# Kernel tuning notes

Hardware: AMD Instinct MI355X
Metric: run time of the kernel (lower is better)

## Reference

```python
import jax, jax.numpy as jnp
import numpy as np

N_NODES = 50000
N_EDGES = 600000
NODE_DIM = 128
HID = 128
NUM_LAYERS = 3


def setup_inputs() -> dict:
    key = jax.random.key(0)
    ks = jax.random.split(key, 16)
    s = lambda fan_in: 1.0 / np.sqrt(fan_in)
    inp = {
        'node_features': jax.random.normal(ks[0], (N_NODES, NODE_DIM), dtype=jnp.float32),
        'edge_index': jax.random.randint(ks[1], (2, N_EDGES), 0, N_NODES, dtype=jnp.int64 if jax.config.jax_enable_x64 else jnp.int32),
        # node embedding
        'W_emb': jax.random.uniform(ks[2], (NODE_DIM, HID), jnp.float32, -s(NODE_DIM), s(NODE_DIM)),
        'b_emb': jnp.zeros((HID,), jnp.float32),
        # gnn layers (stacked over layer axis)
        'W_gnn': jax.random.uniform(ks[3], (NUM_LAYERS, HID, HID), jnp.float32, -s(HID), s(HID)),
        'b_gnn': jnp.zeros((NUM_LAYERS, HID), jnp.float32),
        # edge mask generator
        'W_m1': jax.random.uniform(ks[4], (2 * HID, HID), jnp.float32, -s(2 * HID), s(2 * HID)),
        'b_m1': jnp.zeros((HID,), jnp.float32),
        'W_m2': jax.random.uniform(ks[5], (HID, 1), jnp.float32, -s(HID), s(HID)),
        'b_m2': jnp.zeros((1,), jnp.float32),
        # predictor
        'W_p1': jax.random.uniform(ks[6], (HID, HID), jnp.float32, -s(HID), s(HID)),
        'b_p1': jnp.zeros((HID,), jnp.float32),
        'W_p2': jax.random.uniform(ks[7], (HID, 1), jnp.float32, -s(HID), s(HID)),
        'b_p2': jnp.zeros((1,), jnp.float32),
    }
    return inp


def _edge_mask(h, src, dst, W_m1, b_m1, W_m2, b_m2):
    # per-edge gather + concat -> 2-layer MLP -> sigmoid importance
    ef = jnp.concatenate([h[src], h[dst]], axis=1)          # [E, 2H]
    imp = jax.nn.sigmoid(jax.nn.relu(ef @ W_m1 + b_m1) @ W_m2 + b_m2)[:, 0]  # [E]
    # eval mode: temp=2.0, offset=0.4
    return jax.nn.sigmoid((imp - 0.4) * 2.0)


def reference(node_features, edge_index, W_emb, b_emb, W_gnn, b_gnn,
              W_m1, b_m1, W_m2, b_m2, W_p1, b_p1, W_p2, b_p2):
    src, dst = edge_index[0], edge_index[1]
    n = node_features.shape[0]
    h = jax.nn.relu(node_features @ W_emb + b_emb)           # [N, H]
    mask = _edge_mask(h, src, dst, W_m1, b_m1, W_m2, b_m2)    # [E]
    for i in range(NUM_LAYERS):
        msgs = jax.ops.segment_sum(h[src] * mask[:, None], dst, num_segments=n)  # scatter-add
        h = jax.nn.relu((h + msgs) @ W_gnn[i] + b_gnn[i])
        if i < NUM_LAYERS - 1:
            mask = _edge_mask(h, src, dst, W_m1, b_m1, W_m2, b_m2)
    prediction = jax.nn.relu(h[0] @ W_p1 + b_p1) @ W_p2 + b_p2  # [1]
    return prediction, mask, h
```

## Files before the change

kernel.cpp:

```cpp
#include <hip/hip_runtime.h>
#include <hip/hip_bf16.h>

#define NN 50000
#define NE 600000
#define HD 128
#define DET_SAMPLES 65536
#define NBLK 196
#define NTILES 3125
#define GPERS 782
#define LDT 136

typedef unsigned short ushort_t;
typedef __attribute__((ext_vector_type(8))) short short8v;
typedef __attribute__((ext_vector_type(4))) float f32x4;

__device__ __forceinline__ float sigmoidf_(float x){ return 1.f/(1.f+__expf(-x)); }

__device__ __forceinline__ ushort_t f2bf(float f){
  unsigned int u = __float_as_uint(f);
  unsigned int r = (u + 0x7FFFu + ((u >> 16) & 1u)) >> 16;
  return (ushort_t)r;
}

__device__ __forceinline__ float bflo(unsigned u){ return __uint_as_float(u << 16); }
__device__ __forceinline__ float bfhi(unsigned u){ return __uint_as_float(u & 0xFFFF0000u); }

__global__ void write_scalar_kernel(float* __restrict__ p, float v){ p[0] = v; }

__global__ void detect_kernel(const unsigned int* __restrict__ w, int* __restrict__ flag){
  int i = blockIdx.x*256 + threadIdx.x;
  int z = (w[2*i + 1] == 0u) ? 1 : 0;
  atomicAdd(flag, z);
}

__global__ void extract_kernel(const void* __restrict__ ei, const int* __restrict__ flag,
                               int* __restrict__ srcW, int* __restrict__ dstW,
                               int* __restrict__ counts){
  const int e = blockIdx.x*256 + threadIdx.x;
  if (e >= NE) return;
  int s, d;
  if (*flag > (DET_SAMPLES/2)){
    const long long* p = (const long long*)ei;
    s = (int)p[e]; d = (int)p[NE + e];
  } else {
    const int* p = (const int*)ei;
    s = p[e]; d = p[NE + e];
  }
  srcW[e] = s; dstW[e] = d;
  atomicAdd(&counts[d], 1);
}

__global__ __launch_bounds__(256) void scanA_kernel(const int* __restrict__ counts,
                                                    int* __restrict__ partial){
  __shared__ int s[256];
  const int t = threadIdx.x;
  const int idx = blockIdx.x*256 + t;
  s[t] = (idx < NN) ? counts[idx] : 0;
  __syncthreads();
  for (int off = 128; off > 0; off >>= 1){
    if (t < off) s[t] += s[t + off];
    __syncthreads();
  }
  if (t == 0) partial[blockIdx.x] = s[0];
}

__global__ __launch_bounds__(256) void scanB_kernel(const int* __restrict__ partial,
                                                    int* __restrict__ bOff){
  __shared__ int s[256];
  const int t = threadIdx.x;
  const int v = (t < NBLK) ? partial[t] : 0;
  s[t] = v;
  __syncthreads();
  for (int off = 1; off < 256; off <<= 1){
    int add = (t >= off) ? s[t - off] : 0;
    __syncthreads();
    s[t] += add;
    __syncthreads();
  }
  if (t < NBLK) bOff[t] = s[t] - v;
}

__global__ __launch_bounds__(256) void scanC_kernel(const int* __restrict__ counts,
    const int* __restrict__ bOff, int* __restrict__ row_start, int* __restrict__ cursor){
  __shared__ int s[256];
  const int t = threadIdx.x;
  const int idx = blockIdx.x*256 + t;
  const int c = (idx < NN) ? counts[idx] : 0;
  s[t] = c;
  __syncthreads();
  for (int off = 1; off < 256; off <<= 1){
    int add = (t >= off) ? s[t - off] : 0;
    __syncthreads();
    s[t] += add;
    __syncthreads();
  }
  const int excl = bOff[blockIdx.x] + s[t] - c;
  if (idx < NN){ row_start[idx] = excl; cursor[idx] = excl; }
  else if (idx == NN){ row_start[NN] = excl; }
}

__global__ void fill_kernel(const int* __restrict__ dstI, const int* __restrict__ srcI,
                            int* __restrict__ cursor, int* __restrict__ eids,
                            int* __restrict__ srcS){
  int e = blockIdx.x*256 + threadIdx.x;
  if (e < NE){
    int p = atomicAdd(&cursor[dstI[e]], 1);
    eids[p] = e;
    srcS[p] = srcI[e];
  }
}

__global__ __launch_bounds__(256) void wcvt_all_kernel(const float* __restrict__ Wemb,
    const float* __restrict__ Wgnn, const float* __restrict__ Wm1,
    ushort_t* __restrict__ WtAll){
  const int idx = blockIdx.x*256 + threadIdx.x;
  const int m = idx >> 14;
  const int r = idx & 16383;
  const int k = r >> 7, n = r & 127;
  const float* W = (m == 0) ? Wemb : (m <= 3) ? (Wgnn + (size_t)(m-1)*16384)
                                              : (Wm1  + (size_t)(m-4)*16384);
  WtAll[(size_t)m*16384 + n*HD + k] = f2bf(W[r]);
}

template<int F32A, int DOUV>
__global__ __launch_bounds__(256, 3) void gemm_fused(const void* __restrict__ inP,
    const ushort_t* __restrict__ Wt, const float* __restrict__ bias,
    float* __restrict__ outF, ushort_t* __restrict__ outB,
    const ushort_t* __restrict__ WtU, const ushort_t* __restrict__ WtV,
    const float* __restrict__ biasU, ushort_t* __restrict__ outU,
    ushort_t* __restrict__ outV)
{
  __shared__ ushort_t hT[16*LDT];
  const int cq   = threadIdx.x >> 6;
  const int lane = threadIdx.x & 63;
  const int fr = lane & 15;
  const int fq = lane >> 4;
  short8v bh[4][2];
  #pragma unroll
  for (int ks = 0; ks < 4; ++ks)
    #pragma unroll
    for (int tcl = 0; tcl < 2; ++tcl)
      bh[ks][tcl] = *(const short8v*)(Wt + (size_t)((cq*2+tcl)*16 + fr)*HD + ks*32 + fq*8);
  short8v bu[4][2], bv[4][2];
  if (DOUV){
    #pragma unroll
    for (int ks = 0; ks < 4; ++ks)
      #pragma unroll
      for (int tcl = 0; tcl < 2; ++tcl){
        bu[ks][tcl] = *(const short8v*)(WtU + (size_t)((cq*2+tcl)*16 + fr)*HD + ks*32 + fq*8);
        bv[ks][tcl] = *(const short8v*)(WtV + (size_t)((cq*2+tcl)*16 + fr)*HD + ks*32 + fq*8);
      }
  }
  float bb[2], bub[2];
  #pragma unroll
  for (int tcl = 0; tcl < 2; ++tcl){
    const int col = (cq*2 + tcl)*16 + fr;
    bb[tcl]  = bias ? bias[col] : 0.f;
    bub[tcl] = DOUV ? biasU[col] : 0.f;
  }

  for (int it = 0; it < 4; ++it){
    const int tile = blockIdx.x + it*GPERS;
    if (tile >= NTILES) break;
    const int row0 = tile*16;
    const int arow = row0 + fr;
    f32x4 acc0 = (f32x4)0.0f, acc1 = (f32x4)0.0f;
    #pragma unroll
    for (int ks = 0; ks < 4; ++ks){
      const int k0 = ks*32 + fq*8;
      short8v af;
      if (F32A){
        const float* in = (const float*)inP;
        const float4 a0 = *(const float4*)(in + (size_t)arow*HD + k0);
        const float4 a1 = *(const float4*)(in + (size_t)arow*HD + k0 + 4);
        af[0]=(short)f2bf(a0.x); af[1]=(short)f2bf(a0.y);
        af[2]=(short)f2bf(a0.z); af[3]=(short)f2bf(a0.w);
        af[4]=(short)f2bf(a1.x); af[5]=(short)f2bf(a1.y);
        af[6]=(short)f2bf(a1.z); af[7]=(short)f2bf(a1.w);
      } else {
        const ushort_t* inB = (const ushort_t*)inP;
        af = *(const short8v*)(inB + (size_t)arow*HD + k0);
      }
      acc0 = __builtin_amdgcn_mfma_f32_16x16x32_bf16(af, bh[ks][0], acc0, 0, 0, 0);
      acc1 = __builtin_amdgcn_mfma_f32_16x16x32_bf16(af, bh[ks][1], acc1, 0, 0, 0);
    }
    #pragma unroll
    for (int tcl = 0; tcl < 2; ++tcl){
      const f32x4 a = tcl ? acc1 : acc0;
      const int col = (cq*2 + tcl)*16 + fr;
      #pragma unroll
      for (int j = 0; j < 4; ++j){
        const int r = row0 + fq*4 + j;
        float x = a[j] + bb[tcl];
        x = fmaxf(x, 0.f);
        const ushort_t xb = f2bf(x);
        if (DOUV) hT[(fq*4 + j)*LDT + col] = xb;
        if (outF) outF[(size_t)r*HD + col] = x;
        if (outB) outB[(size_t)r*HD + col] = xb;
      }
    }
    if (DOUV){
      __syncthreads();
      f32x4 aU0 = (f32x4)0.0f, aU1 = (f32x4)0.0f;
      f32x4 aV0 = (f32x4)0.0f, aV1 = (f32x4)0.0f;
      #pragma unroll
      for (int ks = 0; ks < 4; ++ks){
        const short8v af = *(const short8v*)(hT + fr*LDT + ks*32 + fq*8);
        aU0 = __builtin_amdgcn_mfma_f32_16x16x32_bf16(af, bu[ks][0], aU0, 0, 0, 0);
        aU1 = __builtin_amdgcn_mfma_f32_16x16x32_bf16(af, bu[ks][1], aU1, 0, 0, 0);
        aV0 = __builtin_amdgcn_mfma_f32_16x16x32_bf16(af, bv[ks][0], aV0, 0, 0, 0);
        aV1 = __builtin_amdgcn_mfma_f32_16x16x32_bf16(af, bv[ks][1], aV1, 0, 0, 0);
      }
      #pragma unroll
      for (int tcl = 0; tcl < 2; ++tcl){
        const f32x4 u = tcl ? aU1 : aU0;
        const f32x4 v = tcl ? aV1 : aV0;
        const int col = (cq*2 + tcl)*16 + fr;
        #pragma unroll
        for (int j = 0; j < 4; ++j){
          const int r = row0 + fq*4 + j;
          outU[(size_t)r*HD + col] = f2bf(u[j] + bub[tcl]);
          outV[(size_t)r*HD + col] = f2bf(v[j]);
        }
      }
      __syncthreads();
    }
  }
}

__global__ __launch_bounds__(256) void mask_msg_kernel(
    const ushort_t* __restrict__ U, const ushort_t* __restrict__ V,
    const ushort_t* __restrict__ hB,
    ushort_t* __restrict__ hB2,
    const int* __restrict__ srcS, const int* __restrict__ eidS,
    const int* __restrict__ row_start,
    const float* __restrict__ Wm2, const float* __restrict__ bm2,
    float* __restrict__ maskOut)
{
  const int v = blockIdx.x*4 + (threadIdx.x >> 6);
  const int lane = threadIdx.x & 63;
  const int g   = lane >> 4;
  const int sub = lane & 15;
  const float4 wA = ((const float4*)Wm2)[sub*2];
  const float4 wB = ((const float4*)Wm2)[sub*2+1];
  const float b2 = bm2[0];
  const uint4 vv = ((const uint4*)(V + (size_t)v*HD))[sub];
  float a0=0.f,a1=0.f,a2=0.f,a3=0.f,a4=0.f,a5=0.f,a6=0.f,a7=0.f;
  const int beg = row_start[v], end = row_start[v+1];
  int idx = beg + g;
  uint4 uu = make_uint4(0,0,0,0), hh = make_uint4(0,0,0,0);
  int e0 = 0;
  if (idx < end){
    const int s = srcS[idx];
    if (maskOut) e0 = eidS[idx];
    uu = ((const uint4*)(U  + (size_t)s*HD))[sub];
    hh = ((const uint4*)(hB + (size_t)s*HD))[sub];
  }
  while (idx < end){
    const int nidx = idx + 4;
    uint4 uuN = make_uint4(0,0,0,0), hhN = make_uint4(0,0,0,0);
    int eN = 0;
    if (nidx < end){
      const int sn = srcS[nidx];
      if (maskOut) eN = eidS[nidx];
      uuN = ((const uint4*)(U  + (size_t)sn*HD))[sub];
      hhN = ((const uint4*)(hB + (size_t)sn*HD))[sub];
    }
    float p;
    p = fmaxf(bflo(uu.x)+bflo(vv.x), 0.f) * wA.x;
    p = fmaf(fmaxf(bfhi(uu.x)+bfhi(vv.x), 0.f), wA.y, p);
    p = fmaf(fmaxf(bflo(uu.y)+bflo(vv.y), 0.f), wA.z, p);
    p = fmaf(fmaxf(bfhi(uu.y)+bfhi(vv.y), 0.f), wA.w, p);
    p = fmaf(fmaxf(bflo(uu.z)+bflo(vv.z), 0.f), wB.x, p);
    p = fmaf(fmaxf(bfhi(uu.z)+bfhi(vv.z), 0.f), wB.y, p);
    p = fmaf(fmaxf(bflo(uu.w)+bflo(vv.w), 0.f), wB.z, p);
    p = fmaf(fmaxf(bfhi(uu.w)+bfhi(vv.w), 0.f), wB.w, p);
    p += __shfl_xor(p, 1, 64);
    p += __shfl_xor(p, 2, 64);
    p += __shfl_xor(p, 4, 64);
    p += __shfl_xor(p, 8, 64);
    const float imp = sigmoidf_(p + b2);
    const float mk  = sigmoidf_((imp - 0.4f) * 2.0f);
    if (maskOut != nullptr && sub == 0) maskOut[e0] = mk;
    a0 = fmaf(mk, bflo(hh.x), a0);
    a1 = fmaf(mk, bfhi(hh.x), a1);
    a2 = fmaf(mk, bflo(hh.y), a2);
    a3 = fmaf(mk, bfhi(hh.y), a3);
    a4 = fmaf(mk, bflo(hh.z), a4);
    a5 = fmaf(mk, bfhi(hh.z), a5);
    a6 = fmaf(mk, bflo(hh.w), a6);
    a7 = fmaf(mk, bfhi(hh.w), a7);
    uu = uuN; hh = hhN; e0 = eN; idx = nidx;
  }
  a0 += __shfl_xor(a0, 16, 64); a0 += __shfl_xor(a0, 32, 64);
  a1 += __shfl_xor(a1, 16, 64); a1 += __shfl_xor(a1, 32, 64);
  a2 += __shfl_xor(a2, 16, 64); a2 += __shfl_xor(a2, 32, 64);
  a3 += __shfl_xor(a3, 16, 64); a3 += __shfl_xor(a3, 32, 64);
  a4 += __shfl_xor(a4, 16, 64); a4 += __shfl_xor(a4, 32, 64);
  a5 += __shfl_xor(a5, 16, 64); a5 += __shfl_xor(a5, 32, 64);
  a6 += __shfl_xor(a6, 16, 64); a6 += __shfl_xor(a6, 32, 64);
  a7 += __shfl_xor(a7, 16, 64); a7 += __shfl_xor(a7, 32, 64);
  if (g == 0){
    const uint4 hrow = ((const uint4*)(hB + (size_t)v*HD))[sub];
    const float x0 = bflo(hrow.x) + a0, x1 = bfhi(hrow.x) + a1;
    const float x2 = bflo(hrow.y) + a2, x3 = bfhi(hrow.y) + a3;
    const float x4 = bflo(hrow.z) + a4, x5 = bfhi(hrow.z) + a5;
    const float x6 = bflo(hrow.w) + a6, x7 = bfhi(hrow.w) + a7;
    ushort4 p0, p1;
    p0.x = f2bf(x0); p0.y = f2bf(x1); p0.z = f2bf(x2); p0.w = f2bf(x3);
    p1.x = f2bf(x4); p1.y = f2bf(x5); p1.z = f2bf(x6); p1.w = f2bf(x7);
    ushort4* hb2row = (ushort4*)(hB2 + (size_t)v*HD) + sub*2;
    hb2row[0] = p0;
    hb2row[1] = p1;
  }
}

__global__ __launch_bounds__(256, 3) void gemm_final(const ushort_t* __restrict__ inB,
    const ushort_t* __restrict__ Wt, const float* __restrict__ bias,
    float* __restrict__ outF)
{
  const int cq   = threadIdx.x >> 6;
  const int lane = threadIdx.x & 63;
  const int fr = lane & 15;
  const int fq = lane >> 4;
  short8v bh[4][2];
  #pragma unroll
  for (int ks = 0; ks < 4; ++ks)
    #pragma unroll
    for (int tcl = 0; tcl < 2; ++tcl)
      bh[ks][tcl] = *(const short8v*)(Wt + (size_t)((cq*2+tcl)*16 + fr)*HD + ks*32 + fq*8);
  float bb[2];
  #pragma unroll
  for (int tcl = 0; tcl < 2; ++tcl) bb[tcl] = bias[(cq*2 + tcl)*16 + fr];
  for (int it = 0; it < 4; ++it){
    const int tile = blockIdx.x + it*GPERS;
    if (tile >= NTILES) break;
    const int row0 = tile*16;
    const int arow = row0 + fr;
    f32x4 acc0 = (f32x4)0.0f, acc1 = (f32x4)0.0f;
    #pragma unroll
    for (int ks = 0; ks < 4; ++ks){
      const int k0 = ks*32 + fq*8;
      const short8v af = *(const short8v*)(inB + (size_t)arow*HD + k0);
      acc0 = __builtin_amdgcn_mfma_f32_16x16x32_bf16(af, bh[ks][0], acc0, 0, 0, 0);
      acc1 = __builtin_amdgcn_mfma_f32_16x16x32_bf16(af, bh[ks][1], acc1, 0, 0, 0);
    }
    #pragma unroll
    for (int tcl = 0; tcl < 2; ++tcl){
      const f32x4 a = tcl ? acc1 : acc0;
      const int col = (cq*2 + tcl)*16 + fr;
      #pragma unroll
      for (int j = 0; j < 4; ++j){
        const int r = row0 + fq*4 + j;
        outF[(size_t)r*HD + col] = fmaxf(a[j] + bb[tcl], 0.f);
      }
    }
  }
}

__global__ __launch_bounds__(128) void pred_kernel(const float* __restrict__ h,
  const float* __restrict__ Wp1, const float* __restrict__ bp1,
  const float* __restrict__ Wp2, const float* __restrict__ bp2,
  float* __restrict__ out0)
{
  __shared__ float red[128];
  const int t = threadIdx.x;
  float s = bp1[t];
  for (int k = 0; k < HD; ++k) s = fmaf(h[k], Wp1[k*HD + t], s);
  s = fmaxf(s, 0.f) * Wp2[t];
  red[t] = s;
  __syncthreads();
  for (int off = 64; off > 0; off >>= 1){
    if (t < off) red[t] += red[t + off];
    __syncthreads();
  }
  if (t == 0) out0[0] = red[0] + bp2[0];
}

extern "C" void kernel_launch(void* const* d_in, const int* in_sizes, int n_in,
                              void* d_out, int out_size, void* d_ws, size_t ws_size,
                              hipStream_t stream)
{
  (void)out_size;
  float* fOut = (float*)d_out;
  float* predOut = fOut;
  float* maskOut = fOut + 1;
  float* hOut    = fOut + 1 + NE;

  static const int expSizes[14] = {6400000,1200000,16384,128,49152,384,32768,128,128,1,
                                   16384,128,128,1};
  const size_t NEEDED = 87100000;
  float diag = 0.f;
  if (n_in != 14) diag = 900.f + (float)n_in;
  else {
    for (int i = 0; i < 14; ++i)
      if (in_sizes[i] != expSizes[i]){ diag = 200.f + 16.f*(float)i; break; }
  }
  if (diag == 0.f && ws_size < NEEDED) diag = 5000.f + (float)(ws_size >> 20);

  if (diag != 0.f){
    write_scalar_kernel<<<1, 1, 0, stream>>>(predOut, diag);
    return;
  }

  const float* nf   = (const float*)d_in[0];
  const void*  ei   = d_in[1];
  const float* Wemb = (const float*)d_in[2];
  const float* bemb = (const float*)d_in[3];
  const float* Wgnn = (const float*)d_in[4];
  const float* bgnn = (const float*)d_in[5];
  const float* Wm1  = (const float*)d_in[6];
  const float* bm1  = (const float*)d_in[7];
  const float* Wm2  = (const float*)d_in[8];
  const float* bm2  = (const float*)d_in[9];
  const float* Wp1  = (const float*)d_in[10];
  const float* bp1  = (const float*)d_in[11];
  const float* Wp2  = (const float*)d_in[12];
  const float* bp2  = (const float*)d_in[13];

  float* hA    = (float*)d_ws;
  float* tmpU  = hA   + (size_t)NN*HD;
  float* Vbuf  = tmpU + (size_t)NN*HD;
  float* srcSf = Vbuf + (size_t)NN*HD;
  int* srcS    = (int*)srcSf;
  int* row_start = srcS + NE;
  int* cursor  = row_start + (NN + 1);
  int* counts  = cursor + NN;
  int* eids    = counts + NN;
  int* srcW    = eids + NE;
  int* dstW    = srcW + NE;
  int* flag    = dstW + NE;
  int* partial = flag + 1;
  int* bOff    = partial + NBLK;

  ushort_t* Ub  = (ushort_t*)tmpU;
  ushort_t* hB2 = (ushort_t*)tmpU + (size_t)NN*HD;
  ushort_t* Vb  = (ushort_t*)Vbuf;
  ushort_t* hB  = (ushort_t*)Vbuf + (size_t)NN*HD;

  ushort_t* WtAll = (ushort_t*)cursor;
  ushort_t* WtEmb = WtAll;
  ushort_t* WtG0  = WtAll + 1*16384;
  ushort_t* WtG1  = WtAll + 2*16384;
  ushort_t* WtG2  = WtAll + 3*16384;
  ushort_t* WtU   = WtAll + 4*16384;
  ushort_t* WtV   = WtAll + 5*16384;

  hipMemsetAsync(flag, 0, sizeof(int), stream);
  hipMemsetAsync(counts, 0, NN*sizeof(int), stream);
  detect_kernel<<<DET_SAMPLES/256, 256, 0, stream>>>((const unsigned int*)ei, flag);
  extract_kernel<<<(NE + 255)/256, 256, 0, stream>>>(ei, flag, srcW, dstW, counts);

  scanA_kernel<<<NBLK, 256, 0, stream>>>(counts, partial);
  scanB_kernel<<<1, 256, 0, stream>>>(partial, bOff);
  scanC_kernel<<<NBLK, 256, 0, stream>>>(counts, bOff, row_start, cursor);
  fill_kernel<<<(NE + 255)/256, 256, 0, stream>>>(dstW, srcW, cursor, eids, srcS);

  wcvt_all_kernel<<<384, 256, 0, stream>>>(Wemb, Wgnn, Wm1, WtAll);

  gemm_fused<1,1><<<GPERS, 256, 0, stream>>>(nf, WtEmb, bemb, nullptr, hB,
                                             WtU, WtV, bm1, Ub, Vb);

  const ushort_t* WtG[3] = {WtG0, WtG1, WtG2};
  for (int L = 0; L < 3; ++L){
    float* mOut = (L < 2) ? nullptr : maskOut;
    mask_msg_kernel<<<NN/4, 256, 0, stream>>>(Ub, Vb, hB, hB2, srcS, eids, row_start,
                                              Wm2, bm2, mOut);
    if (L < 2){
      gemm_fused<0,1><<<GPERS, 256, 0, stream>>>(hB2, WtG[L], bgnn + (size_t)L*HD,
                                                 nullptr, hB, WtU, WtV, bm1, Ub, Vb);
    } else {
      gemm_final<<<GPERS, 256, 0, stream>>>(hB2, WtG[2], bgnn + 2*HD, hOut);
    }
  }

  pred_kernel<<<1, 128, 0, stream>>>(hOut, Wp1, bp1, Wp2, bp2, predOut);
}
```

Baseline: 372.3 us.

## Prefetch next GEMM A-tile into registers and fold int64 detection into extract

The int64/int32 edge-index detection now runs inside the extract kernel using a per-block shared flag, which removes a memset, a detect kernel launch and a global atomic. The fused and final GEMM kernels now load the next tile's A fragment into registers while the current tile's MFMAs and epilogue run, hiding global load latency. The per-block detection is less robust: a block whose high words are all zero for int32 data would be misread as int64. Holding the prefetched fragments also raises register pressure.

```diff
diff --git a/kernel.cpp b/kernel.cpp
--- a/kernel.cpp
+++ b/kernel.cpp
@@ -4,7 +4,6 @@
 #define NN 50000
 #define NE 600000
 #define HD 128
-#define DET_SAMPLES 65536
 #define NBLK 196
 #define NTILES 3125
 #define GPERS 782
@@ -27,27 +26,30 @@
 
 __global__ void write_scalar_kernel(float* __restrict__ p, float v){ p[0] = v; }
 
-__global__ void detect_kernel(const unsigned int* __restrict__ w, int* __restrict__ flag){
-  int i = blockIdx.x*256 + threadIdx.x;
-  int z = (w[2*i + 1] == 0u) ? 1 : 0;
-  atomicAdd(flag, z);
-}
-
-__global__ void extract_kernel(const void* __restrict__ ei, const int* __restrict__ flag,
-                               int* __restrict__ srcW, int* __restrict__ dstW,
-                               int* __restrict__ counts){
+__global__ __launch_bounds__(256) void extract_kernel(const void* __restrict__ ei,
+    int* __restrict__ srcW, int* __restrict__ dstW, int* __restrict__ counts){
+  __shared__ int hasNZ;
   const int e = blockIdx.x*256 + threadIdx.x;
-  if (e >= NE) return;
-  int s, d;
-  if (*flag > (DET_SAMPLES/2)){
-    const long long* p = (const long long*)ei;
-    s = (int)p[e]; d = (int)p[NE + e];
-  } else {
-    const int* p = (const int*)ei;
-    s = p[e]; d = p[NE + e];
-  }
-  srcW[e] = s; dstW[e] = d;
-  atomicAdd(&counts[d], 1);
+  if (threadIdx.x == 0) hasNZ = 0;
+  __syncthreads();
+  if (e < NE){
+    const unsigned* w = (const unsigned*)ei;
+    if (w[2*(size_t)e + 1] != 0u) hasNZ = 1;
+  }
+  __syncthreads();
+  const bool is64 = (hasNZ == 0);
+  if (e < NE){
+    int s, d;
+    if (is64){
+      const long long* p = (const long long*)ei;
+      s = (int)p[e]; d = (int)p[NE + e];
+    } else {
+      const int* p = (const int*)ei;
+      s = p[e]; d = p[NE + e];
+    }
+    srcW[e] = s; dstW[e] = d;
+    atomicAdd(&counts[d], 1);
+  }
 }
 
 __global__ __launch_bounds__(256) void scanA_kernel(const int* __restrict__ counts,
@@ -159,30 +161,64 @@
     bub[tcl] = DOUV ? biasU[col] : 0.f;
   }
 
+  float4  aF[8];
+  short8v aB[4];
+  {
+    const int arow = blockIdx.x*16 + fr;
+    if (F32A){
+      const float* in = (const float*)inP;
+      #pragma unroll
+      for (int ks = 0; ks < 4; ++ks){
+        aF[2*ks]   = *(const float4*)(in + (size_t)arow*HD + ks*32 + fq*8);
+        aF[2*ks+1] = *(const float4*)(in + (size_t)arow*HD + ks*32 + fq*8 + 4);
+      }
+    } else {
+      const ushort_t* inB = (const ushort_t*)inP;
+      #pragma unroll
+      for (int ks = 0; ks < 4; ++ks)
+        aB[ks] = *(const short8v*)(inB + (size_t)arow*HD + ks*32 + fq*8);
+    }
+  }
+
+  #pragma unroll
   for (int it = 0; it < 4; ++it){
     const int tile = blockIdx.x + it*GPERS;
     if (tile >= NTILES) break;
     const int row0 = tile*16;
-    const int arow = row0 + fr;
     f32x4 acc0 = (f32x4)0.0f, acc1 = (f32x4)0.0f;
     #pragma unroll
     for (int ks = 0; ks < 4; ++ks){
-      const int k0 = ks*32 + fq*8;
       short8v af;
       if (F32A){
-        const float* in = (const float*)inP;
-        const float4 a0 = *(const float4*)(in + (size_t)arow*HD + k0);
-        const float4 a1 = *(const float4*)(in + (size_t)arow*HD + k0 + 4);
+        const float4 a0 = aF[2*ks], a1 = aF[2*ks+1];
         af[0]=(short)f2bf(a0.x); af[1]=(short)f2bf(a0.y);
         af[2]=(short)f2bf(a0.z); af[3]=(short)f2bf(a0.w);
         af[4]=(short)f2bf(a1.x); af[5]=(short)f2bf(a1.y);
         af[6]=(short)f2bf(a1.z); af[7]=(short)f2bf(a1.w);
       } else {
-        const ushort_t* inB = (const ushort_t*)inP;
-        af = *(const short8v*)(inB + (size_t)arow*HD + k0);
+        af = aB[ks];
       }
       acc0 = __builtin_amdgcn_mfma_f32_16x16x32_bf16(af, bh[ks][0], acc0, 0, 0, 0);
       acc1 = __builtin_amdgcn_mfma_f32_16x16x32_bf16(af, bh[ks][1], acc1, 0, 0, 0);
+    }
+    {
+      const int ntile = tile + GPERS;
+      if (ntile < NTILES){
+        const int arow = ntile*16 + fr;
+        if (F32A){
+          const float* in = (const float*)inP;
+          #pragma unroll
+          for (int ks = 0; ks < 4; ++ks){
+            aF[2*ks]   = *(const float4*)(in + (size_t)arow*HD + ks*32 + fq*8);
+            aF[2*ks+1] = *(const float4*)(in + (size_t)arow*HD + ks*32 + fq*8 + 4);
+          }
+        } else {
+          const ushort_t* inB = (const ushort_t*)inP;
+          #pragma unroll
+          for (int ks = 0; ks < 4; ++ks)
+            aB[ks] = *(const short8v*)(inB + (size_t)arow*HD + ks*32 + fq*8);
+        }
+      }
     }
     #pragma unroll
     for (int tcl = 0; tcl < 2; ++tcl){
@@ -191,8 +227,7 @@
       #pragma unroll
       for (int j = 0; j < 4; ++j){
         const int r = row0 + fq*4 + j;
-        float x = a[j] + bb[tcl];
-        x = fmaxf(x, 0.f);
+        float x = fmaxf(a[j] + bb[tcl], 0.f);
         const ushort_t xb = f2bf(x);
         if (DOUV) hT[(fq*4 + j)*LDT + col] = xb;
         if (outF) outF[(size_t)r*HD + col] = x;
@@ -224,6 +259,61 @@
         }
       }
       __syncthreads();
+    }
+  }
+}
+
+__global__ __launch_bounds__(256, 3) void gemm_final(const ushort_t* __restrict__ inB,
+    const ushort_t* __restrict__ Wt, const float* __restrict__ bias,
+    float* __restrict__ outF)
+{
+  const int cq   = threadIdx.x >> 6;
+  const int lane = threadIdx.x & 63;
+  const int fr = lane & 15;
+  const int fq = lane >> 4;
+  short8v bh[4][2];
+  #pragma unroll
+  for (int ks = 0; ks < 4; ++ks)
+    #pragma unroll
+    for (int tcl = 0; tcl < 2; ++tcl)
+      bh[ks][tcl] = *(const short8v*)(Wt + (size_t)((cq*2+tcl)*16 + fr)*HD + ks*32 + fq*8);
+  float bb[2];
+  #pragma unroll
+  for (int tcl = 0; tcl < 2; ++tcl) bb[tcl] = bias[(cq*2 + tcl)*16 + fr];
+  short8v aB[4];
+  {
+    const int arow = blockIdx.x*16 + fr;
+    #pragma unroll
+    for (int ks = 0; ks < 4; ++ks)
+      aB[ks] = *(const short8v*)(inB + (size_t)arow*HD + ks*32 + fq*8);
+  }
+  #pragma unroll
+  for (int it = 0; it < 4; ++it){
+    const int tile = blockIdx.x + it*GPERS;
+    if (tile >= NTILES) break;
+    const int row0 = tile*16;
+    f32x4 acc0 = (f32x4)0.0f, acc1 = (f32x4)0.0f;
+    #pragma unroll
+    for (int ks = 0; ks < 4; ++ks){
+      acc0 = __builtin_amdgcn_mfma_f32_16x16x32_bf16(aB[ks], bh[ks][0], acc0, 0, 0, 0);
+      acc1 = __builtin_amdgcn_mfma_f32_16x16x32_bf16(aB[ks], bh[ks][1], acc1, 0, 0, 0);
+    }
+    const int ntile = tile + GPERS;
+    if (ntile < NTILES){
+      const int arow = ntile*16 + fr;
+      #pragma unroll
+      for (int ks = 0; ks < 4; ++ks)
+        aB[ks] = *(const short8v*)(inB + (size_t)arow*HD + ks*32 + fq*8);
+    }
+    #pragma unroll
+    for (int tcl = 0; tcl < 2; ++tcl){
+      const f32x4 a = tcl ? acc1 : acc0;
+      const int col = (cq*2 + tcl)*16 + fr;
+      #pragma unroll
+      for (int j = 0; j < 4; ++j){
+        const int r = row0 + fq*4 + j;
+        outF[(size_t)r*HD + col] = fmaxf(a[j] + bb[tcl], 0.f);
+      }
     }
   }
 }
@@ -315,49 +405,6 @@
   }
 }
 
-__global__ __launch_bounds__(256, 3) void gemm_final(const ushort_t* __restrict__ inB,
-    const ushort_t* __restrict__ Wt, const float* __restrict__ bias,
-    float* __restrict__ outF)
-{
-  const int cq   = threadIdx.x >> 6;
-  const int lane = threadIdx.x & 63;
-  const int fr = lane & 15;
-  const int fq = lane >> 4;
-  short8v bh[4][2];
-  #pragma unroll
-  for (int ks = 0; ks < 4; ++ks)
-    #pragma unroll
-    for (int tcl = 0; tcl < 2; ++tcl)
-      bh[ks][tcl] = *(const short8v*)(Wt + (size_t)((cq*2+tcl)*16 + fr)*HD + ks*32 + fq*8);
-  float bb[2];
-  #pragma unroll
-  for (int tcl = 0; tcl < 2; ++tcl) bb[tcl] = bias[(cq*2 + tcl)*16 + fr];
-  for (int it = 0; it < 4; ++it){
-    const int tile = blockIdx.x + it*GPERS;
-    if (tile >= NTILES) break;
-    const int row0 = tile*16;
-    const int arow = row0 + fr;
-    f32x4 acc0 = (f32x4)0.0f, acc1 = (f32x4)0.0f;
-    #pragma unroll
-    for (int ks = 0; ks < 4; ++ks){
-      const int k0 = ks*32 + fq*8;
-      const short8v af = *(const short8v*)(inB + (size_t)arow*HD + k0);
-      acc0 = __builtin_amdgcn_mfma_f32_16x16x32_bf16(af, bh[ks][0], acc0, 0, 0, 0);
-      acc1 = __builtin_amdgcn_mfma_f32_16x16x32_bf16(af, bh[ks][1], acc1, 0, 0, 0);
-    }
-    #pragma unroll
-    for (int tcl = 0; tcl < 2; ++tcl){
-      const f32x4 a = tcl ? acc1 : acc0;
-      const int col = (cq*2 + tcl)*16 + fr;
-      #pragma unroll
-      for (int j = 0; j < 4; ++j){
-        const int r = row0 + fq*4 + j;
-        outF[(size_t)r*HD + col] = fmaxf(a[j] + bb[tcl], 0.f);
-      }
-    }
-  }
-}
-
 __global__ __launch_bounds__(128) void pred_kernel(const float* __restrict__ h,
   const float* __restrict__ Wp1, const float* __restrict__ bp1,
   const float* __restrict__ Wp2, const float* __restrict__ bp2,
@@ -446,10 +493,8 @@
   ushort_t* WtU   = WtAll + 4*16384;
   ushort_t* WtV   = WtAll + 5*16384;
 
-  hipMemsetAsync(flag, 0, sizeof(int), stream);
   hipMemsetAsync(counts, 0, NN*sizeof(int), stream);
-  detect_kernel<<<DET_SAMPLES/256, 256, 0, stream>>>((const unsigned int*)ei, flag);
-  extract_kernel<<<(NE + 255)/256, 256, 0, stream>>>(ei, flag, srcW, dstW, counts);
+  extract_kernel<<<(NE + 255)/256, 256, 0, stream>>>(ei, srcW, dstW, counts);
 
   scanA_kernel<<<NBLK, 256, 0, stream>>>(counts, partial);
   scanB_kernel<<<1, 256, 0, stream>>>(partial, bOff);
```

Result: faster. 356.8 us (-4.2%).
